# Kernel optimization log

Hardware: AMD Instinct MI355X
Metric: run time of the kernel (lower is better)

The kernel has to match this reference:

```python
import jax, jax.numpy as jnp
import numpy as np

TEMPERATURE = 0.5
NEG_INF = -1e30


def setup_inputs() -> dict:
    key = jax.random.key(0)
    batch_size, k, d = 2048, 4, 256
    features = jax.random.normal(key, (batch_size * k, d), dtype=jnp.float32)
    return {"features": features, "batch_size": batch_size, "k": k}


def reference(features, batch_size, k):
    n = batch_size * k
    f = features.reshape(n, -1)
    f = f / jnp.linalg.norm(f, axis=1, keepdims=True)
    sim = jnp.matmul(f, f.T) / TEMPERATURE  # [N, N]

    gid = jnp.arange(n) // k
    eye = jnp.eye(n, dtype=bool)
    pos_mask = (gid[:, None] == gid[None, :]) & ~eye  # same image, not self
    all_mask = ~eye  # positives + negatives (everything except self)

    lse_pos = jax.nn.logsumexp(jnp.where(pos_mask, sim, NEG_INF), axis=1)
    lse_all = jax.nn.logsumexp(jnp.where(all_mask, sim, NEG_INF), axis=1)
    # every row has k-1 >= 1 positives, so all queries contribute
    return jnp.mean(-(lse_pos - lse_all))
```

## Files before the change

kernel.cpp:

```cpp
#include <hip/hip_runtime.h>
#include <math.h>

#define NROW 8192
#define DIM 256
#define NTILE 64
#define NBLK 2080

typedef float f32x4  __attribute__((ext_vector_type(4)));
typedef short short8 __attribute__((ext_vector_type(8)));

__device__ __forceinline__ ushort f2bf_rne(float x) {
    unsigned u = __float_as_uint(x);
    unsigned r = (u + 0x7FFFu + ((u >> 16) & 1u)) >> 16;
    return (ushort)r;
}
__device__ __forceinline__ float bf2f(ushort h) {
    return __uint_as_float(((unsigned)h) << 16);
}

__global__ void zero_kernel(float* __restrict__ p, int n) {
    int i = blockIdx.x * blockDim.x + threadIdx.x;
    if (i < n) p[i] = 0.0f;
}

__global__ __launch_bounds__(256) void prep_kernel(const float* __restrict__ f,
                                                   ushort* __restrict__ Hi,
                                                   ushort* __restrict__ Lo) {
    const int row = blockIdx.x * 4 + (threadIdx.x >> 6);
    const int l   = threadIdx.x & 63;
    float4 v = reinterpret_cast<const float4*>(f + (size_t)row * DIM)[l];
    float ss = v.x * v.x + v.y * v.y + v.z * v.z + v.w * v.w;
#pragma unroll
    for (int m = 32; m; m >>= 1) ss += __shfl_xor(ss, m, 64);
    const float inv = 1.0f / sqrtf(ss);
    float xv[4] = {v.x * inv, v.y * inv, v.z * inv, v.w * inv};
    ushort hv[4], lv[4];
#pragma unroll
    for (int i = 0; i < 4; ++i) {
        hv[i] = f2bf_rne(xv[i]);
        lv[i] = f2bf_rne(xv[i] - bf2f(hv[i]));
    }
    size_t idx = (size_t)((row >> 4) * 32 + (l >> 1)) * 128 + (row & 15) * 8 + (l & 1) * 4;
    *reinterpret_cast<ushort4*>(&Hi[idx]) = make_ushort4(hv[0], hv[1], hv[2], hv[3]);
    *reinterpret_cast<ushort4*>(&Lo[idx]) = make_ushort4(lv[0], lv[1], lv[2], lv[3]);
}

__device__ __forceinline__ void gload16(const void* g, void* lp) {
    __builtin_amdgcn_global_load_lds((__attribute__((address_space(1))) void*)g,
                                     (__attribute__((address_space(3))) void*)lp, 16, 0, 0);
}

__global__ __launch_bounds__(256, 3) void infonce_mfma(const ushort* __restrict__ Hi,
                                                       const ushort* __restrict__ Lo,
                                                       float* __restrict__ all_sum,
                                                       float* __restrict__ pos_sum) {
    __shared__ ushort lds[2][2][4096];

    int ti = 0, rem = blockIdx.x;
    while (rem >= NTILE - ti) { rem -= NTILE - ti; ++ti; }
    const int tj = ti + rem;

    const int tid = threadIdx.x;
    const int wid = tid >> 6, l = tid & 63;
    const int wr = wid >> 1, wc = wid & 1;

    f32x4 acc[4][4];
#pragma unroll
    for (int m = 0; m < 4; ++m)
#pragma unroll
        for (int n = 0; n < 4; ++n) acc[m][n] = (f32x4){0.f, 0.f, 0.f, 0.f};

#define STAGE(buf, s) do {                                                              \
        const int pass_ = (s) >> 3, kk_ = (s) & 7;                                      \
        const ushort* As_ = (pass_ == 2) ? Lo : Hi;                                     \
        const ushort* Bs_ = (pass_ == 1) ? Lo : Hi;                                     \
        const int f0_ = wid * 2, f1_ = f0_ + 1;                                         \
        gload16(&As_[(size_t)((ti * 8 + f0_) * 4096 + kk_ * 512) + l * 8],              \
                &lds[buf][0][f0_ * 512 + l * 8]);                                       \
        gload16(&As_[(size_t)((ti * 8 + f1_) * 4096 + kk_ * 512) + l * 8],              \
                &lds[buf][0][f1_ * 512 + l * 8]);                                       \
        gload16(&Bs_[(size_t)((tj * 8 + f0_) * 4096 + kk_ * 512) + l * 8],              \
                &lds[buf][1][f0_ * 512 + l * 8]);                                       \
        gload16(&Bs_[(size_t)((tj * 8 + f1_) * 4096 + kk_ * 512) + l * 8],              \
                &lds[buf][1][f1_ * 512 + l * 8]);                                       \
    } while (0)

#define COMPUTE(buf) do {                                                               \
        short8 af_[4], bf_[4];                                                          \
        _Pragma("unroll") for (int m = 0; m < 4; ++m)                                   \
            af_[m] = *reinterpret_cast<const short8*>(&lds[buf][0][(wr * 4 + m) * 512 + l * 8]); \
        _Pragma("unroll") for (int n = 0; n < 4; ++n)                                   \
            bf_[n] = *reinterpret_cast<const short8*>(&lds[buf][1][(wc * 4 + n) * 512 + l * 8]); \
        _Pragma("unroll") for (int m = 0; m < 4; ++m)                                   \
            _Pragma("unroll") for (int n = 0; n < 4; ++n)                               \
                acc[m][n] = __builtin_amdgcn_mfma_f32_16x16x32_bf16(af_[m], bf_[n], acc[m][n], 0, 0, 0); \
    } while (0)

    STAGE(0, 0);
#pragma unroll 2
    for (int s = 0; s < 24; ++s) {
        if (s < 23) STAGE((s + 1) & 1, s + 1);
        __syncthreads();
        COMPUTE(s & 1);
        __syncthreads();
    }

    const int rbase = ti * 128 + wr * 64;
    const int cbase = tj * 128 + wc * 64;
    const int h = l >> 4, c16 = l & 15;

    if (ti == tj) {
#pragma unroll
        for (int m = 0; m < 4; ++m)
#pragma unroll
            for (int e = 0; e < 4; ++e) {
                const int row = rbase + m * 16 + h * 4 + e;
                float asum = 0.f, psum = 0.f;
#pragma unroll
                for (int n = 0; n < 4; ++n) {
                    const int col = cbase + n * 16 + c16;
                    float v = __expf(2.0f * acc[m][n][e]);
                    v = (row == col) ? 0.f : v;
                    asum += v;
                    psum += ((row >> 2) == (col >> 2)) ? v : 0.f;
                }
#pragma unroll
                for (int mk = 1; mk < 16; mk <<= 1) {
                    asum += __shfl_xor(asum, mk, 64);
                    psum += __shfl_xor(psum, mk, 64);
                }
                if (c16 == 0) {
                    atomicAdd(&all_sum[row], asum);
                    atomicAdd(&pos_sum[row], psum);
                }
            }
    } else {
        float csum[4] = {0.f, 0.f, 0.f, 0.f};
#pragma unroll
        for (int m = 0; m < 4; ++m)
#pragma unroll
            for (int e = 0; e < 4; ++e) {
                const int row = rbase + m * 16 + h * 4 + e;
                float asum = 0.f;
#pragma unroll
                for (int n = 0; n < 4; ++n) {
                    float v = __expf(2.0f * acc[m][n][e]);
                    asum += v;
                    csum[n] += v;
                }
#pragma unroll
                for (int mk = 1; mk < 16; mk <<= 1) asum += __shfl_xor(asum, mk, 64);
                if (c16 == 0) atomicAdd(&all_sum[row], asum);
            }
#pragma unroll
        for (int n = 0; n < 4; ++n) {
            float cs = csum[n];
            cs += __shfl_xor(cs, 16, 64);
            cs += __shfl_xor(cs, 32, 64);
            if (h == 0) atomicAdd(&all_sum[cbase + n * 16 + c16], cs);
        }
    }
#undef STAGE
#undef COMPUTE
}

__global__ void loss_kernel(const float* __restrict__ all_sum,
                            const float* __restrict__ pos_sum,
                            float* __restrict__ out) {
    const int tid = threadIdx.x;
    float s = 0.0f;
    for (int i = tid; i < NROW; i += 256)
        s += logf(all_sum[i]) - logf(pos_sum[i]);
#pragma unroll
    for (int off = 32; off; off >>= 1) s += __shfl_xor(s, off, 64);
    __shared__ float red[4];
    if ((tid & 63) == 0) red[tid >> 6] = s;
    __syncthreads();
    if (tid == 0) out[0] = (red[0] + red[1] + red[2] + red[3]) / (float)NROW;
}

extern "C" void kernel_launch(void* const* d_in, const int* in_sizes, int n_in,
                              void* d_out, int out_size, void* d_ws, size_t ws_size,
                              hipStream_t stream) {
    const float* f = (const float*)d_in[0];
    float* out = (float*)d_out;

    float*  all_sum = (float*)d_ws;
    float*  pos_sum = all_sum + NROW;
    ushort* Hi      = (ushort*)(pos_sum + NROW);
    ushort* Lo      = Hi + (size_t)NROW * DIM;

    zero_kernel<<<64, 256, 0, stream>>>(all_sum, 2 * NROW);
    prep_kernel<<<NROW / 4, 256, 0, stream>>>(f, Hi, Lo);
    infonce_mfma<<<NBLK, 256, 0, stream>>>(Hi, Lo, all_sum, pos_sum);
    loss_kernel<<<1, 256, 0, stream>>>(all_sum, pos_sum, out);
}
```

Before: 160.1 us.

## Triple-buffer MFMA k-loop with single barrier, fuse zeroing into prep

Replaces the double-buffered k-loop, which had two __syncthreads per step, with a three-buffer pipeline. Loads are issued two stages ahead, completion is tracked with explicit vmcnt waits, each step uses one barrier, and MFMA issue priority is raised. The separate zero kernel is removed by having prep_kernel clear the sum buffers. The loss kernel is widened to 1024 threads and uses fast log. Risks are a hand-managed waitcnt/barrier ordering and more LDS use, which may affect occupancy.

```diff
diff --git a/kernel.cpp b/kernel.cpp
--- a/kernel.cpp
+++ b/kernel.cpp
@@ -5,6 +5,7 @@
 #define DIM 256
 #define NTILE 64
 #define NBLK 2080
+#define NT 24
 
 typedef float f32x4  __attribute__((ext_vector_type(4)));
 typedef short short8 __attribute__((ext_vector_type(8)));
@@ -18,14 +19,11 @@
     return __uint_as_float(((unsigned)h) << 16);
 }
 
-__global__ void zero_kernel(float* __restrict__ p, int n) {
-    int i = blockIdx.x * blockDim.x + threadIdx.x;
-    if (i < n) p[i] = 0.0f;
-}
-
 __global__ __launch_bounds__(256) void prep_kernel(const float* __restrict__ f,
                                                    ushort* __restrict__ Hi,
-                                                   ushort* __restrict__ Lo) {
+                                                   ushort* __restrict__ Lo,
+                                                   float* __restrict__ sums) {
+    if (threadIdx.x < 8) sums[blockIdx.x * 8 + threadIdx.x] = 0.0f;
     const int row = blockIdx.x * 4 + (threadIdx.x >> 6);
     const int l   = threadIdx.x & 63;
     float4 v = reinterpret_cast<const float4*>(f + (size_t)row * DIM)[l];
@@ -54,7 +52,7 @@
                                                        const ushort* __restrict__ Lo,
                                                        float* __restrict__ all_sum,
                                                        float* __restrict__ pos_sum) {
-    __shared__ ushort lds[2][2][4096];
+    __shared__ ushort lds[3][2][4096];
 
     int ti = 0, rem = blockIdx.x;
     while (rem >= NTILE - ti) { rem -= NTILE - ti; ++ti; }
@@ -70,39 +68,49 @@
 #pragma unroll
         for (int n = 0; n < 4; ++n) acc[m][n] = (f32x4){0.f, 0.f, 0.f, 0.f};
 
-#define STAGE(buf, s) do {                                                              \
-        const int pass_ = (s) >> 3, kk_ = (s) & 7;                                      \
+#define STAGE(bufi, t) do {                                                             \
+        const int pass_ = (t) >> 3, kk_ = (t) & 7;                                      \
         const ushort* As_ = (pass_ == 2) ? Lo : Hi;                                     \
         const ushort* Bs_ = (pass_ == 1) ? Lo : Hi;                                     \
         const int f0_ = wid * 2, f1_ = f0_ + 1;                                         \
         gload16(&As_[(size_t)((ti * 8 + f0_) * 4096 + kk_ * 512) + l * 8],              \
-                &lds[buf][0][f0_ * 512 + l * 8]);                                       \
+                &lds[bufi][0][f0_ * 512 + l * 8]);                                      \
         gload16(&As_[(size_t)((ti * 8 + f1_) * 4096 + kk_ * 512) + l * 8],              \
-                &lds[buf][0][f1_ * 512 + l * 8]);                                       \
+                &lds[bufi][0][f1_ * 512 + l * 8]);                                      \
         gload16(&Bs_[(size_t)((tj * 8 + f0_) * 4096 + kk_ * 512) + l * 8],              \
-                &lds[buf][1][f0_ * 512 + l * 8]);                                       \
+                &lds[bufi][1][f0_ * 512 + l * 8]);                                      \
         gload16(&Bs_[(size_t)((tj * 8 + f1_) * 4096 + kk_ * 512) + l * 8],              \
-                &lds[buf][1][f1_ * 512 + l * 8]);                                       \
+                &lds[bufi][1][f1_ * 512 + l * 8]);                                      \
     } while (0)
 
-#define COMPUTE(buf) do {                                                               \
+#define VWAIT(n) asm volatile("s_waitcnt vmcnt(" #n ")" ::: "memory")
+
+#define BODY(t, bR, bS) do {                                                            \
         short8 af_[4], bf_[4];                                                          \
         _Pragma("unroll") for (int m = 0; m < 4; ++m)                                   \
-            af_[m] = *reinterpret_cast<const short8*>(&lds[buf][0][(wr * 4 + m) * 512 + l * 8]); \
+            af_[m] = *reinterpret_cast<const short8*>(&lds[bR][0][(wr * 4 + m) * 512 + l * 8]); \
         _Pragma("unroll") for (int n = 0; n < 4; ++n)                                   \
-            bf_[n] = *reinterpret_cast<const short8*>(&lds[buf][1][(wc * 4 + n) * 512 + l * 8]); \
+            bf_[n] = *reinterpret_cast<const short8*>(&lds[bR][1][(wc * 4 + n) * 512 + l * 8]); \
+        if ((t) + 2 < NT) STAGE(bS, (t) + 2);                                           \
+        __builtin_amdgcn_s_setprio(1);                                                  \
         _Pragma("unroll") for (int m = 0; m < 4; ++m)                                   \
             _Pragma("unroll") for (int n = 0; n < 4; ++n)                               \
                 acc[m][n] = __builtin_amdgcn_mfma_f32_16x16x32_bf16(af_[m], bf_[n], acc[m][n], 0, 0, 0); \
+        __builtin_amdgcn_s_setprio(0);                                                  \
+        if ((t) + 2 < NT) { VWAIT(4); } else { VWAIT(0); }                              \
+        __builtin_amdgcn_s_barrier();                                                   \
     } while (0)
 
     STAGE(0, 0);
-#pragma unroll 2
-    for (int s = 0; s < 24; ++s) {
-        if (s < 23) STAGE((s + 1) & 1, s + 1);
-        __syncthreads();
-        COMPUTE(s & 1);
-        __syncthreads();
+    STAGE(1, 1);
+    VWAIT(4);
+    __builtin_amdgcn_s_barrier();
+
+#pragma unroll 1
+    for (int tb = 0; tb < NT; tb += 3) {
+        BODY(tb + 0, 0, 2);
+        BODY(tb + 1, 1, 0);
+        BODY(tb + 2, 2, 1);
     }
 
     const int rbase = ti * 128 + wr * 64;
@@ -161,22 +169,31 @@
         }
     }
 #undef STAGE
-#undef COMPUTE
-}
-
-__global__ void loss_kernel(const float* __restrict__ all_sum,
-                            const float* __restrict__ pos_sum,
-                            float* __restrict__ out) {
+#undef VWAIT
+#undef BODY
+}
+
+__global__ __launch_bounds__(1024) void loss_kernel(const float* __restrict__ all_sum,
+                                                    const float* __restrict__ pos_sum,
+                                                    float* __restrict__ out) {
     const int tid = threadIdx.x;
     float s = 0.0f;
-    for (int i = tid; i < NROW; i += 256)
-        s += logf(all_sum[i]) - logf(pos_sum[i]);
+#pragma unroll
+    for (int r = 0; r < 8; ++r) {
+        const int i = tid + r * 1024;
+        s += __logf(all_sum[i]) - __logf(pos_sum[i]);
+    }
 #pragma unroll
     for (int off = 32; off; off >>= 1) s += __shfl_xor(s, off, 64);
-    __shared__ float red[4];
+    __shared__ float red[16];
     if ((tid & 63) == 0) red[tid >> 6] = s;
     __syncthreads();
-    if (tid == 0) out[0] = (red[0] + red[1] + red[2] + red[3]) / (float)NROW;
+    if (tid == 0) {
+        float tot = 0.f;
+#pragma unroll
+        for (int i = 0; i < 16; ++i) tot += red[i];
+        out[0] = tot / (float)NROW;
+    }
 }
 
 extern "C" void kernel_launch(void* const* d_in, const int* in_sizes, int n_in,
@@ -190,8 +207,7 @@
     ushort* Hi      = (ushort*)(pos_sum + NROW);
     ushort* Lo      = Hi + (size_t)NROW * DIM;
 
-    zero_kernel<<<64, 256, 0, stream>>>(all_sum, 2 * NROW);
-    prep_kernel<<<NROW / 4, 256, 0, stream>>>(f, Hi, Lo);
+    prep_kernel<<<NROW / 4, 256, 0, stream>>>(f, Hi, Lo, all_sum);
     infonce_mfma<<<NBLK, 256, 0, stream>>>(Hi, Lo, all_sum, pos_sum);
-    loss_kernel<<<1, 256, 0, stream>>>(all_sum, pos_sum, out);
-}
+    loss_kernel<<<1, 1024, 0, stream>>>(all_sum, pos_sum, out);
+}
```

After: 141.6 us. -11.5%, faster.
